# Kernel tuning notes

Measured on AMD Instinct MI355X. Metric: run time of the kernel, lower is better.

## Reference

```python
import jax, jax.numpy as jnp
import numpy as np

TEMP_LEN = 16
TARGET_LEN = 22
DIM = 768
HEADS = 12
B = 16
NT = TEMP_LEN * TEMP_LEN          # 256 template tokens
NG = TARGET_LEN * TARGET_LEN      # 484 target tokens
N = NT + NG                       # 740
POS_HID = 512


def _gaussian_heatmap(center, size, sig=1.0):
    x_axis = np.linspace(0, size[0] - 1, size[0]) - center[0]
    y_axis = np.linspace(0, size[1] - 1, size[1]) - center[1]
    xx, yy = np.meshgrid(x_axis, y_axis)
    return np.exp(-0.5 * (xx ** 2 + yy ** 2) / sig ** 2)


def _bias_index(L):
    # faithful to getBiasIndex (w_len == h_len here)
    coords = np.stack(np.meshgrid(np.arange(L), np.arange(L), indexing='ij'))  # [2,L,L]
    flat = coords.reshape(2, -1)                                               # [2,L*L]
    rel = (flat[:, :, None] - flat[:, None, :]).transpose(1, 2, 0).astype(np.int64)
    rel[:, :, 0] += L - 1
    rel[:, :, 1] += L - 1
    rel[:, :, 0] *= 2 * L - 1
    return rel.sum(-1)  # [L*L, L*L]


def setup_inputs() -> dict:
    key = jax.random.key(0)
    ks = jax.random.split(key, 12)
    f32 = jnp.float32
    x = jax.random.normal(ks[0], (B, N, DIM), dtype=f32)
    temp_q = jax.random.normal(ks[1], (B, NT, DIM), dtype=f32)
    target_q = jax.random.normal(ks[2], (B, NG, DIM), dtype=f32)
    # linear weights stored [in, out] (transposed torch layout)
    w = lambda k, i, o: jax.random.normal(k, (i, o), dtype=f32) * 0.02
    q_w = w(ks[3], DIM, DIM)
    k_w = w(ks[4], DIM, DIM)
    v_w = w(ks[5], DIM, DIM)
    proj_w = w(ks[6], DIM, DIM)
    proj_b = jnp.zeros((DIM,), dtype=f32)
    rpb_table = jax.random.normal(ks[7], ((2 * TARGET_LEN - 1) ** 2, HEADS), dtype=f32) * 0.0002
    rpb_table_temp = jax.random.normal(ks[8], ((2 * TEMP_LEN - 1) ** 2, HEADS), dtype=f32) * 0.0002
    pos_w1 = w(ks[9], 2, POS_HID)
    pos_b1 = jnp.zeros((POS_HID,), dtype=f32)
    pos_w2 = w(ks[10], POS_HID, HEADS)
    pos_b2 = jnp.zeros((HEADS,), dtype=f32)
    # deterministic cross-bias coordinate table (non-learned buffer)
    temp_tab = _gaussian_heatmap((TEMP_LEN // 2, TEMP_LEN // 2), (TEMP_LEN, TEMP_LEN)).astype(np.float32).flatten() \
        + np.linspace(-0.2, 0.2, NT, dtype=np.float32)
    targ_tab = _gaussian_heatmap((TARGET_LEN // 2, TARGET_LEN // 2), (TARGET_LEN, TARGET_LEN)).astype(np.float32).flatten() \
        + np.linspace(-0.2, 0.2, NG, dtype=np.float32)
    # torch.meshgrid default indexing='ij': [2, NT, NG] -> permute(1,2,0) -> [NT,NG,2]
    temp_target = np.stack(np.meshgrid(temp_tab, targ_tab, indexing='ij')).transpose(1, 2, 0)
    target_temp_tab = jnp.asarray(temp_target.transpose(1, 0, 2))  # [NG, NT, 2]
    temp_idx = jnp.asarray(_bias_index(TEMP_LEN))       # [NT, NT] int64
    target_idx = jnp.asarray(_bias_index(TARGET_LEN))   # [NG, NG] int64
    return {
        'x': x, 'temp_q': temp_q, 'target_q': target_q,
        'q_w': q_w, 'k_w': k_w, 'v_w': v_w, 'proj_w': proj_w, 'proj_b': proj_b,
        'rpb_table': rpb_table, 'rpb_table_temp': rpb_table_temp,
        'pos_w1': pos_w1, 'pos_b1': pos_b1, 'pos_w2': pos_w2, 'pos_b2': pos_b2,
        'target_temp_tab': target_temp_tab,
        'temp_idx': temp_idx, 'target_idx': target_idx,
    }


def reference(x, temp_q, target_q, q_w, k_w, v_w, proj_w, proj_b,
              rpb_table, rpb_table_temp, pos_w1, pos_b1, pos_w2, pos_b2,
              target_temp_tab, temp_idx, target_idx):
    Bsz, Ntok, C = x.shape
    H = HEADS
    hd = C // H
    scale = hd ** -0.5

    q_in = jnp.concatenate([temp_q, target_q], axis=1)                 # [B,N,C]
    q = (q_in @ q_w).reshape(Bsz, Ntok, H, hd).transpose(0, 2, 1, 3)   # [B,H,N,hd]
    k = (x @ k_w).reshape(Bsz, Ntok, H, hd).transpose(0, 2, 1, 3)
    v = (x @ v_w).reshape(Bsz, Ntok, H, hd).transpose(0, 2, 1, 3)

    # gathered relative position biases -> [H, Ni, Ni]
    temp_rpb = rpb_table_temp[temp_idx.reshape(-1)].reshape(NT, NT, H).transpose(2, 0, 1)
    targ_rpb = rpb_table[target_idx.reshape(-1)].reshape(NG, NG, H).transpose(2, 0, 1)
    # MLP cross bias: [NG, NT, 2] -> [NG, NT, H] -> [H, NG, NT]
    hid = jax.nn.relu(target_temp_tab @ pos_w1 + pos_b1)
    target_temp_bias = (hid @ pos_w2 + pos_b2).transpose(2, 0, 1)      # [H,NG,NT]
    temp_target_bias = target_temp_bias.transpose(0, 2, 1)             # [H,NT,NG]
    top = jnp.concatenate([temp_rpb, temp_target_bias], axis=2)        # [H,NT,N]
    bot = jnp.concatenate([target_temp_bias, targ_rpb], axis=2)        # [H,NG,N]
    bias = jnp.concatenate([top, bot], axis=1)[None]                   # [1,H,N,N]

    attn = jnp.einsum('bhnd,bhmd->bhnm', q, k) * scale + bias
    attn = jax.nn.softmax(attn, axis=-1)
    out = jnp.einsum('bhnm,bhmd->bhnd', attn, v).transpose(0, 2, 1, 3).reshape(Bsz, Ntok, C)
    return out @ proj_w + proj_b
```

## Files before the change

kernel.cpp:

```cpp
#include <hip/hip_runtime.h>


typedef unsigned short u16;
typedef short bf16x8 __attribute__((ext_vector_type(8)));
typedef float f32x4 __attribute__((ext_vector_type(4)));

#define BSZ   16
#define NTOK  740
#define NTMP  256
#define NTGT  484
#define DIMC  768
#define NHEAD 12
#define HDIM  64
#define MROWS (BSZ*NTOK)
#define LOG2E 1.44269504f
#define NEGS  (-23.0831032f)

__device__ __forceinline__ float bflo(unsigned int u) {
    return __uint_as_float(u << 16);
}
__device__ __forceinline__ float bfhi(unsigned int u) {
    return __uint_as_float(u & 0xffff0000u);
}
__device__ __forceinline__ u16 f2bf(float f) {
    unsigned int u = __float_as_uint(f);
    u += 0x7fffu + ((u >> 16) & 1u);
    return (u16)(u >> 16);
}

__device__ __forceinline__ void gl_lds16(const u16* g, u16* l) {
    __builtin_amdgcn_global_load_lds(
        (const __attribute__((address_space(1))) unsigned int*)(unsigned long long)g,
        (__attribute__((address_space(3))) unsigned int*)(unsigned int)(unsigned long long)l,
        16, 0, 0);
}

__device__ __forceinline__ size_t b2off(int h, int i, int j) {
    return ((size_t)(h * NTOK + i)) * 768 + ((j >> 6) << 6) + ((j & 15) << 2) + ((j >> 4) & 3);
}

#define PREP_MLP  484
#define PREP_TRW  (PREP_MLP + 576)
#define PREP_ALL  (PREP_TRW + 2220)

__global__ __launch_bounds__(256) void prep_kernel(
    const float* __restrict__ w0, const float* __restrict__ w1,
    const float* __restrict__ w2, const float* __restrict__ w3,
    u16* __restrict__ Wt,
    const float* __restrict__ rpb, const float* __restrict__ rpbt,
    const int* __restrict__ tidx, const int* __restrict__ gidx,
    const float* __restrict__ pw1, const float* __restrict__ pb1,
    const float* __restrict__ pw2, const float* __restrict__ pb2,
    const float* __restrict__ tab, u16* __restrict__ bias)
{
    __shared__ float T[64][65];
    const int blk = blockIdx.x;
    const int tid = threadIdx.x;

    if (blk < PREP_MLP) {
        int g = blk;
        int t = tid;
        float a  = tab[(g * NTMP + t) * 2 + 0];
        float bb = tab[(g * NTMP + t) * 2 + 1];
        float acc[NHEAD];
        #pragma unroll
        for (int h = 0; h < NHEAD; h++) acc[h] = pb2[h];
        for (int k = 0; k < 512; k++) {
            float hid = fmaxf(a * pw1[k] + bb * pw1[512 + k] + pb1[k], 0.0f);
            #pragma unroll
            for (int h = 0; h < NHEAD; h++) acc[h] += hid * pw2[k * NHEAD + h];
        }
        #pragma unroll
        for (int h = 0; h < NHEAD; h++) {
            u16 v = f2bf(acc[h] * LOG2E);
            bias[b2off(h, t, NTMP + g)] = v;
            bias[b2off(h, NTMP + g, t)] = v;
        }
    } else if (blk < PREP_TRW) {
        int t = blk - PREP_MLP;
        int z = t / 144, rem = t - z * 144;
        int bx = rem % 12, by = rem / 12;
        const float* src = (z == 0) ? w0 : (z == 1) ? w1 : (z == 2) ? w2 : w3;
        const float scale = (z == 0) ? 0.125f * LOG2E : 1.0f;
        u16* dst = Wt + (size_t)z * DIMC * DIMC;
        int out0 = bx * 64, in0 = by * 64;
        #pragma unroll
        for (int l = 0; l < 4; l++) {
            int u = tid + (l << 8);
            int r = u >> 4, c4 = (u & 15) << 2;
            float4 p = *(const float4*)(src + (size_t)(in0 + r) * DIMC + out0 + c4);
            T[r][c4] = p.x; T[r][c4 + 1] = p.y; T[r][c4 + 2] = p.z; T[r][c4 + 3] = p.w;
        }
        __syncthreads();
        #pragma unroll
        for (int l = 0; l < 2; l++) {
            int u = tid + (l << 8);
            int r = u >> 3, c8 = (u & 7) << 3;
            u16 e[8];
            #pragma unroll
            for (int i = 0; i < 8; i++) e[i] = f2bf(T[c8 + i][r] * scale);
            *(uint4*)(dst + (size_t)(out0 + r) * DIMC + in0 + c8) = *(uint4*)e;
        }
    } else {
        int t = blk - PREP_TRW;
        int jb = t % 3, i = t / 3;
        int j = jb * 256 + tid;
        u16 vals[NHEAD];
        if (j >= NTOK) {
            u16 neg = f2bf(-1e30f);
            #pragma unroll
            for (int h = 0; h < NHEAD; h++) vals[h] = neg;
        } else if (i < NTMP && j < NTMP) {
            int idx = tidx[i * NTMP + j];
            #pragma unroll
            for (int h = 0; h < NHEAD; h++) vals[h] = f2bf(rpbt[idx * NHEAD + h] * LOG2E);
        } else if (i >= NTMP && j >= NTMP) {
            int idx = gidx[(i - NTMP) * NTGT + (j - NTMP)];
            #pragma unroll
            for (int h = 0; h < NHEAD; h++) vals[h] = f2bf(rpb[idx * NHEAD + h] * LOG2E);
        } else {
            return;
        }
        #pragma unroll
        for (int h = 0; h < NHEAD; h++) bias[b2off(h, i, j)] = vals[h];
    }
}

__global__ __launch_bounds__(256) void gemm_qkv(
    const float* __restrict__ x, const float* __restrict__ tq,
    const float* __restrict__ gq, const u16* __restrict__ Wt,
    u16* __restrict__ Qo, u16* __restrict__ Ko, u16* __restrict__ Vo)
{
    __shared__ __align__(16) u16 As[4096];
    __shared__ __align__(16) u16 Bs0[8192];
    __shared__ __align__(16) u16 Bs1[8192];
    const int tid = threadIdx.x;
    const int lane = tid & 63, w = tid >> 6;
    const int quad = lane >> 4, ln = lane & 15;

    const int nwg = 12 * 185;
    const int flat = blockIdx.y * 12 + blockIdx.x;
    const int q = nwg >> 3, r = nwg & 7;
    const int xcd = flat & 7, sidx = flat >> 3;
    const int wg = (xcd < r) ? xcd * (q + 1) + sidx
                             : r * (q + 1) + (xcd - r) * q + sidx;
    const int by = wg / 12, bx = wg - by * 12;

    const int m0 = by << 6;
    const int wm = (w >> 1) << 5, wn = (w & 1) << 6;

    const int rr = tid >> 2, qq = tid & 3;
    const int arow = m0 + rr;

    if (bx < 6) {
        const int nn = bx << 7;
        const u16* Wb = Wt + (size_t)nn * DIMC;
        int b = arow / NTOK, n = arow - b * NTOK;
        const float* aptr = (n < NTMP)
                          ? tq + ((size_t)(b * NTMP + n)) * DIMC
                          : gq + ((size_t)(b * NTGT + (n - NTMP))) * DIMC;

        f32x4 acc[2][4];
        #pragma unroll
        for (int i = 0; i < 2; i++)
            #pragma unroll
            for (int j = 0; j < 4; j++) acc[i][j] = (f32x4){0.f, 0.f, 0.f, 0.f};

        #pragma unroll 1
        for (int t = 0; t < 12; t++) {
            const int k0 = t << 6;
            __syncthreads();
            const float* s = aptr + k0 + (qq << 4);
            float4 a0 = ((const float4*)s)[0], a1 = ((const float4*)s)[1];
            float4 a2 = ((const float4*)s)[2], a3 = ((const float4*)s)[3];
            #pragma unroll
            for (int l = 0; l < 4; l++) {
                int f = tid + (l << 8);
                int c8 = f >> 7, r2 = f & 127;
                gl_lds16(Wb + (size_t)r2 * DIMC + k0 + c8 * 8, &Bs0[f * 8]);
            }
            u16 e[16] = {f2bf(a0.x), f2bf(a0.y), f2bf(a0.z), f2bf(a0.w),
                         f2bf(a1.x), f2bf(a1.y), f2bf(a1.z), f2bf(a1.w),
                         f2bf(a2.x), f2bf(a2.y), f2bf(a2.z), f2bf(a2.w),
                         f2bf(a3.x), f2bf(a3.y), f2bf(a3.z), f2bf(a3.w)};
            *(uint4*)&As[(((qq << 1) + 0) * 64 + rr) * 8] = ((uint4*)e)[0];
            *(uint4*)&As[(((qq << 1) + 1) * 64 + rr) * 8] = ((uint4*)e)[1];
            __syncthreads();
            #pragma unroll
            for (int kp = 0; kp < 2; kp++) {
                bf16x8 af[2], bfr[4];
                #pragma unroll
                for (int mt = 0; mt < 2; mt++)
                    af[mt] = *(const bf16x8*)
                        &As[(((kp << 2) + quad) * 64 + wm + mt * 16 + ln) * 8];
                #pragma unroll
                for (int nt = 0; nt < 4; nt++)
                    bfr[nt] = *(const bf16x8*)
                        &Bs0[(((kp << 2) + quad) * 128 + wn + nt * 16 + ln) * 8];
                #pragma unroll
                for (int mt = 0; mt < 2; mt++)
                    #pragma unroll
                    for (int nt = 0; nt < 4; nt++)
                        acc[mt][nt] = __builtin_amdgcn_mfma_f32_16x16x32_bf16(
                            af[mt], bfr[nt], acc[mt][nt], 0, 0, 0);
            }
        }
        #pragma unroll
        for (int mt = 0; mt < 2; mt++)
            #pragma unroll
            for (int reg = 0; reg < 4; reg++) {
                int grow = m0 + wm + mt * 16 + (quad << 2) + reg;
                #pragma unroll
                for (int nt = 0; nt < 4; nt++)
                    Qo[(size_t)grow * DIMC + nn + wn + nt * 16 + ln]
                        = f2bf(acc[mt][nt][reg]);
            }
    } else {
        const int nn = (bx - 6) << 7;
        const u16* Wbk = Wt + (size_t)DIMC * DIMC + (size_t)nn * DIMC;
        const u16* Wbv = Wt + 2 * (size_t)DIMC * DIMC + (size_t)nn * DIMC;
        const float* aptr = x + (size_t)arow * DIMC;

        f32x4 ak[2][4], av[2][4];
        #pragma unroll
        for (int i = 0; i < 2; i++)
            #pragma unroll
            for (int j = 0; j < 4; j++) {
                ak[i][j] = (f32x4){0.f, 0.f, 0.f, 0.f};
                av[i][j] = (f32x4){0.f, 0.f, 0.f, 0.f};
            }

        #pragma unroll 1
        for (int t = 0; t < 12; t++) {
            const int k0 = t << 6;
            __syncthreads();
            const float* s = aptr + k0 + (qq << 4);
            float4 a0 = ((const float4*)s)[0], a1 = ((const float4*)s)[1];
            float4 a2 = ((const float4*)s)[2], a3 = ((const float4*)s)[3];
            #pragma unroll
            for (int l = 0; l < 4; l++) {
                int f = tid + (l << 8);
                int c8 = f >> 7, r2 = f & 127;
                gl_lds16(Wbk + (size_t)r2 * DIMC + k0 + c8 * 8, &Bs0[f * 8]);
                gl_lds16(Wbv + (size_t)r2 * DIMC + k0 + c8 * 8, &Bs1[f * 8]);
            }
            u16 e[16] = {f2bf(a0.x), f2bf(a0.y), f2bf(a0.z), f2bf(a0.w),
                         f2bf(a1.x), f2bf(a1.y), f2bf(a1.z), f2bf(a1.w),
                         f2bf(a2.x), f2bf(a2.y), f2bf(a2.z), f2bf(a2.w),
                         f2bf(a3.x), f2bf(a3.y), f2bf(a3.z), f2bf(a3.w)};
            *(uint4*)&As[(((qq << 1) + 0) * 64 + rr) * 8] = ((uint4*)e)[0];
            *(uint4*)&As[(((qq << 1) + 1) * 64 + rr) * 8] = ((uint4*)e)[1];
            __syncthreads();
            #pragma unroll
            for (int kp = 0; kp < 2; kp++) {
                bf16x8 af[2], bk[4], bv[4];
                #pragma unroll
                for (int mt = 0; mt < 2; mt++)
                    af[mt] = *(const bf16x8*)
                        &As[(((kp << 2) + quad) * 64 + wm + mt * 16 + ln) * 8];
                #pragma unroll
                for (int nt = 0; nt < 4; nt++) {
                    bk[nt] = *(const bf16x8*)
                        &Bs0[(((kp << 2) + quad) * 128 + wn + nt * 16 + ln) * 8];
                    bv[nt] = *(const bf16x8*)
                        &Bs1[(((kp << 2) + quad) * 128 + wn + nt * 16 + ln) * 8];
                }
                #pragma unroll
                for (int mt = 0; mt < 2; mt++)
                    #pragma unroll
                    for (int nt = 0; nt < 4; nt++) {
                        ak[mt][nt] = __builtin_amdgcn_mfma_f32_16x16x32_bf16(
                            af[mt], bk[nt], ak[mt][nt], 0, 0, 0);
                        av[mt][nt] = __builtin_amdgcn_mfma_f32_16x16x32_bf16(
                            af[mt], bv[nt], av[mt][nt], 0, 0, 0);
                    }
            }
        }
        #pragma unroll
        for (int mt = 0; mt < 2; mt++)
            #pragma unroll
            for (int reg = 0; reg < 4; reg++) {
                int grow = m0 + wm + mt * 16 + (quad << 2) + reg;
                #pragma unroll
                for (int nt = 0; nt < 4; nt++) {
                    int gcol = nn + wn + nt * 16 + ln;
                    Ko[(size_t)grow * DIMC + gcol] = f2bf(ak[mt][nt][reg]);
                    Vo[(size_t)grow * DIMC + gcol] = f2bf(av[mt][nt][reg]);
                }
            }
    }
}

__global__ __launch_bounds__(256) void gemm_proj(
    const u16* __restrict__ A, const u16* __restrict__ Wt,
    const float* __restrict__ pb, float* __restrict__ Cf)
{
    __shared__ __align__(16) u16 As[4096];
    __shared__ __align__(16) u16 Bs[8192];
    const int tid = threadIdx.x;
    const int lane = tid & 63, w = tid >> 6;
    const int quad = lane >> 4, ln = lane & 15;

    const int nwg = 6 * 185;
    const int flat = blockIdx.y * 6 + blockIdx.x;
    const int q = nwg >> 3, r = nwg & 7;
    const int xcd = flat & 7, sidx = flat >> 3;
    const int wg = (xcd < r) ? xcd * (q + 1) + sidx
                             : r * (q + 1) + (xcd - r) * q + sidx;
    const int by = wg / 6, bx = wg - by * 6;

    const int m0 = by << 6;
    const int wm = (w >> 1) << 5, wn = (w & 1) << 6;
    const int nn = bx << 7;
    const u16* Wb = Wt + (size_t)nn * DIMC;

    f32x4 acc[2][4];
    #pragma unroll
    for (int i = 0; i < 2; i++)
        #pragma unroll
        for (int j = 0; j < 4; j++) acc[i][j] = (f32x4){0.f, 0.f, 0.f, 0.f};

    #pragma unroll 1
    for (int t = 0; t < 12; t++) {
        __syncthreads();
        const int k0 = t << 6;
        #pragma unroll
        for (int l = 0; l < 2; l++) {
            int f = tid + (l << 8);
            int c8 = f >> 6, r2 = f & 63;
            gl_lds16(A + (size_t)(m0 + r2) * DIMC + k0 + c8 * 8, &As[f * 8]);
        }
        #pragma unroll
        for (int l = 0; l < 4; l++) {
            int f = tid + (l << 8);
            int c8 = f >> 7, r2 = f & 127;
            gl_lds16(Wb + (size_t)r2 * DIMC + k0 + c8 * 8, &Bs[f * 8]);
        }
        __syncthreads();
        #pragma unroll
        for (int kp = 0; kp < 2; kp++) {
            bf16x8 af[2], bfr[4];
            #pragma unroll
            for (int mt = 0; mt < 2; mt++)
                af[mt] = *(const bf16x8*)
                    &As[(((kp << 2) + quad) * 64 + wm + mt * 16 + ln) * 8];
            #pragma unroll
            for (int nt = 0; nt < 4; nt++)
                bfr[nt] = *(const bf16x8*)
                    &Bs[(((kp << 2) + quad) * 128 + wn + nt * 16 + ln) * 8];
            #pragma unroll
            for (int mt = 0; mt < 2; mt++)
                #pragma unroll
                for (int nt = 0; nt < 4; nt++)
                    acc[mt][nt] = __builtin_amdgcn_mfma_f32_16x16x32_bf16(
                        af[mt], bfr[nt], acc[mt][nt], 0, 0, 0);
        }
    }

    #pragma unroll
    for (int mt = 0; mt < 2; mt++)
        #pragma unroll
        for (int reg = 0; reg < 4; reg++) {
            int grow = m0 + wm + mt * 16 + (quad << 2) + reg;
            #pragma unroll
            for (int nt = 0; nt < 4; nt++) {
                int gcol = nn + wn + nt * 16 + ln;
                Cf[(size_t)grow * DIMC + gcol] = acc[mt][nt][reg] + pb[gcol];
            }
        }
}

__global__ __launch_bounds__(256) void attn_mfma(
    const u16* __restrict__ Qg, const u16* __restrict__ Kg,
    const u16* __restrict__ Vg, const u16* __restrict__ bias,
    u16* __restrict__ ctx)
{
    __shared__ __align__(16) u16 KsL[4096];
    __shared__ __align__(16) u16 VtL[64 * 72];
    __shared__ __align__(16) u16 Pw[4][16][72];

    const int tid = threadIdx.x;
    const int lane = tid & 63, w = tid >> 6;
    const int quad = lane >> 4, ln = lane & 15;

    const int flat = (blockIdx.z * 12 + blockIdx.y) * 12 + blockIdx.x;
    const int wg = (flat & 7) * 288 + (flat >> 3);
    const int h = wg / 192;
    const int rem = wg - h * 192;
    const int b = rem / 12;
    const int q0 = (rem - b * 12) << 6;

    const int mbase = q0 + (w << 4);
    const u16* bp = bias + ((size_t)h * NTOK) * 768;

    bf16x8 aq[2];
    {
        int qrow = mbase + ln; if (qrow >= NTOK) qrow = NTOK - 1;
        #pragma unroll
        for (int kp = 0; kp < 2; kp++)
            aq[kp] = *(const bf16x8*)(Qg + ((size_t)(b * NTOK + qrow)) * DIMC
                                      + h * HDIM + kp * 32 + (quad << 3));
    }
    int boff[4];
    #pragma unroll
    for (int reg = 0; reg < 4; reg++) {
        int rr = mbase + (quad << 2) + reg;
        if (rr >= NTOK) rr = NTOK - 1;
        boff[reg] = rr * 768 + (ln << 2);
    }

    const int pswz = ((ln >> 2) & 3) << 4;

    float rs[4] = {};
    f32x4 O[4];
    #pragma unroll
    for (int dt = 0; dt < 4; dt++) O[dt] = (f32x4){0.f, 0.f, 0.f, 0.f};

    for (int j0 = 0; j0 < NTOK; j0 += 64) {
        __syncthreads();
        #pragma unroll
        for (int l = 0; l < 2; l++) {
            int f = tid + (l << 8);
            int chunk = f >> 6, jr = f & 63;
            int krow = j0 + jr; if (krow >= NTOK) krow = NTOK - 1;
            gl_lds16(Kg + ((size_t)(b * NTOK + krow)) * DIMC + h * HDIM + chunk * 8,
                     KsL + f * 8);
        }
        uint2 bvv[4];
        #pragma unroll
        for (int reg = 0; reg < 4; reg++)
            bvv[reg] = *(const uint2*)(bp + boff[reg] + j0);
        #pragma unroll
        for (int l = 0; l < 2; l++) {
            int u = tid + (l << 8);
            int jr = u >> 3, d0 = (u & 7) << 3;
            int vrow = j0 + jr; if (vrow >= NTOK) vrow = NTOK - 1;
            uint4 p = *(const uint4*)(Vg + ((size_t)(b * NTOK + vrow)) * DIMC + h * HDIM + d0);
            const u16* pe = (const u16*)&p;
            int jswz = jr ^ d0;
            #pragma unroll
            for (int i = 0; i < 8; i++) VtL[(d0 + i) * 72 + jswz] = pe[i];
        }
        __syncthreads();

        bf16x8 bv[4][2];
        #pragma unroll
        for (int dt = 0; dt < 4; dt++) {
            int key8 = ((dt * 2 + (ln >> 3)) & 7) << 3;
            #pragma unroll
            for (int kp = 0; kp < 2; kp++) {
                int koff = (kp * 32 + (quad << 3)) ^ key8;
                bv[dt][kp] = *(const bf16x8*)&VtL[(dt * 16 + ln) * 72 + koff];
            }
        }

        f32x4 s[4];
        #pragma unroll
        for (int nt = 0; nt < 4; nt++) s[nt] = (f32x4){NEGS, NEGS, NEGS, NEGS};
        __builtin_amdgcn_s_setprio(1);
        #pragma unroll
        for (int kp = 0; kp < 2; kp++)
            #pragma unroll
            for (int nt = 0; nt < 4; nt++) {
                bf16x8 bk = *(const bf16x8*)
                    &KsL[(((kp << 2) + quad) * 64 + nt * 16 + ln) * 8];
                s[nt] = __builtin_amdgcn_mfma_f32_16x16x32_bf16(aq[kp], bk, s[nt], 0, 0, 0);
            }
        __builtin_amdgcn_s_setprio(0);

        #pragma unroll
        for (int reg = 0; reg < 4; reg++) {
            uint2 bb = bvv[reg];
            float p0 = __builtin_exp2f(s[0][reg] + bflo(bb.x));
            float p1 = __builtin_exp2f(s[1][reg] + bfhi(bb.x));
            float p2 = __builtin_exp2f(s[2][reg] + bflo(bb.y));
            float p3 = __builtin_exp2f(s[3][reg] + bfhi(bb.y));
            s[0][reg] = p0; s[1][reg] = p1;
            s[2][reg] = p2; s[3][reg] = p3;
            rs[reg] += p0 + p1 + p2 + p3;
        }
        u16* pwb = &Pw[w][0][0];
        #pragma unroll
        for (int nt = 0; nt < 4; nt++) {
            int colw = ((nt ^ quad) << 4) + ln;
            #pragma unroll
            for (int reg = 0; reg < 4; reg++)
                pwb[((quad << 2) + reg) * 72 + colw] = f2bf(s[nt][reg]);
        }
        bf16x8 ap[2];
        #pragma unroll
        for (int kp = 0; kp < 2; kp++) {
            int koff = (kp * 32 + (quad << 3)) ^ pswz;
            ap[kp] = *(const bf16x8*)&pwb[ln * 72 + koff];
        }
        __builtin_amdgcn_s_setprio(1);
        #pragma unroll
        for (int dt = 0; dt < 4; dt++)
            #pragma unroll
            for (int kp = 0; kp < 2; kp++)
                O[dt] = __builtin_amdgcn_mfma_f32_16x16x32_bf16(
                    ap[kp], bv[dt][kp], O[dt], 0, 0, 0);
        __builtin_amdgcn_s_setprio(0);
    }

    #pragma unroll
    for (int reg = 0; reg < 4; reg++) {
        float t = rs[reg];
        #pragma unroll
        for (int mk = 8; mk >= 1; mk >>= 1) t += __shfl_xor(t, mk);
        float inv = 1.0f / t;
        int row = mbase + (quad << 2) + reg;
        if (row < NTOK) {
            #pragma unroll
            for (int dt = 0; dt < 4; dt++)
                ctx[((size_t)(b * NTOK + row)) * DIMC + h * HDIM + dt * 16 + ln]
                    = f2bf(O[dt][reg] * inv);
        }
    }
}

extern "C" void kernel_launch(void* const* d_in, const int* in_sizes, int n_in,
                              void* d_out, int out_size, void* d_ws, size_t ws_size,
                              hipStream_t stream)
{
    const float* x        = (const float*)d_in[0];
    const float* temp_q   = (const float*)d_in[1];
    const float* target_q = (const float*)d_in[2];
    const float* q_w      = (const float*)d_in[3];
    const float* k_w      = (const float*)d_in[4];
    const float* v_w      = (const float*)d_in[5];
    const float* proj_w   = (const float*)d_in[6];
    const float* proj_b   = (const float*)d_in[7];
    const float* rpb      = (const float*)d_in[8];
    const float* rpbt     = (const float*)d_in[9];
    const float* pw1      = (const float*)d_in[10];
    const float* pb1      = (const float*)d_in[11];
    const float* pw2      = (const float*)d_in[12];
    const float* pb2      = (const float*)d_in[13];
    const float* tab      = (const float*)d_in[14];
    const int*   tidx     = (const int*)d_in[15];
    const int*   gidx     = (const int*)d_in[16];
    float* out = (float*)d_out;

    char* ws = (char*)d_ws;
    const size_t S = (size_t)MROWS * DIMC * sizeof(u16);
    const size_t SZB = (size_t)NHEAD * NTOK * 768 * sizeof(u16);
    u16* CTX   = (u16*)(ws);
    u16* V     = (u16*)(ws + S);
    u16* Q     = (u16*)(ws + 2 * S);
    u16* K     = (u16*)(ws + 3 * S);
    u16* BIAS2 = (u16*)(ws + 4 * S);
    u16* WT    = (u16*)(ws + 4 * S + SZB);

    prep_kernel<<<dim3(PREP_ALL), 256, 0, stream>>>(
        q_w, k_w, v_w, proj_w, WT,
        rpb, rpbt, tidx, gidx,
        pw1, pb1, pw2, pb2, tab, BIAS2);

    const u16* WTp = WT + 3 * (size_t)DIMC * DIMC;

    gemm_qkv<<<dim3(12, 185), 256, 0, stream>>>(x, temp_q, target_q, WT, Q, K, V);
    attn_mfma<<<dim3(12, 12, 16), 256, 0, stream>>>(Q, K, V, BIAS2, CTX);
    gemm_proj<<<dim3(6, 185), 256, 0, stream>>>(CTX, WTp, proj_b, out);
}
```

Measured before the change: 473.2 us.

## Split fused K/V GEMM blocks into uniform Q/K/V tiles with swizzled A LDS

The QKV projection kernel no longer has half its blocks compute both K and V. Every block now computes one 64x128 tile of Q, K or V, on an 18x185 grid. This halves the accumulators and B-tile LDS per block, adds a launch-bounds occupancy hint, and balances work across blocks. The A tile in LDS gets an XOR swizzle to cut bank conflicts. The cost is that each K/V block now reloads and reconverts the fp32 x rows that the fused version shared between K and V.

Result: no change. 470.7 us (-0.5%).

```diff
diff --git a/kernel.cpp b/kernel.cpp
--- a/kernel.cpp
+++ b/kernel.cpp
@@ -126,169 +126,104 @@
     }
 }
 
-__global__ __launch_bounds__(256) void gemm_qkv(
+__global__ __launch_bounds__(256, 6) void gemm_qkv(
     const float* __restrict__ x, const float* __restrict__ tq,
     const float* __restrict__ gq, const u16* __restrict__ Wt,
     u16* __restrict__ Qo, u16* __restrict__ Ko, u16* __restrict__ Vo)
 {
     __shared__ __align__(16) u16 As[4096];
-    __shared__ __align__(16) u16 Bs0[8192];
-    __shared__ __align__(16) u16 Bs1[8192];
+    __shared__ __align__(16) u16 Bs[8192];
     const int tid = threadIdx.x;
     const int lane = tid & 63, w = tid >> 6;
     const int quad = lane >> 4, ln = lane & 15;
 
-    const int nwg = 12 * 185;
-    const int flat = blockIdx.y * 12 + blockIdx.x;
+    const int nwg = 18 * 185;
+    const int flat = blockIdx.y * 18 + blockIdx.x;
     const int q = nwg >> 3, r = nwg & 7;
     const int xcd = flat & 7, sidx = flat >> 3;
     const int wg = (xcd < r) ? xcd * (q + 1) + sidx
                              : r * (q + 1) + (xcd - r) * q + sidx;
-    const int by = wg / 12, bx = wg - by * 12;
+    const int by = wg / 18, bx = wg - by * 18;
 
     const int m0 = by << 6;
     const int wm = (w >> 1) << 5, wn = (w & 1) << 6;
 
+    const int p = (bx < 6) ? 0 : (bx < 12) ? 1 : 2;
+    const int nn = (bx - p * 6) << 7;
+    const u16* Wb = Wt + (size_t)p * DIMC * DIMC + (size_t)nn * DIMC;
+    u16* Co = (p == 0) ? Qo : (p == 1) ? Ko : Vo;
+
     const int rr = tid >> 2, qq = tid & 3;
     const int arow = m0 + rr;
-
-    if (bx < 6) {
-        const int nn = bx << 7;
-        const u16* Wb = Wt + (size_t)nn * DIMC;
+    const float* aptr;
+    if (p == 0) {
         int b = arow / NTOK, n = arow - b * NTOK;
-        const float* aptr = (n < NTMP)
-                          ? tq + ((size_t)(b * NTMP + n)) * DIMC
-                          : gq + ((size_t)(b * NTGT + (n - NTMP))) * DIMC;
-
-        f32x4 acc[2][4];
-        #pragma unroll
-        for (int i = 0; i < 2; i++)
-            #pragma unroll
-            for (int j = 0; j < 4; j++) acc[i][j] = (f32x4){0.f, 0.f, 0.f, 0.f};
-
-        #pragma unroll 1
-        for (int t = 0; t < 12; t++) {
-            const int k0 = t << 6;
-            __syncthreads();
-            const float* s = aptr + k0 + (qq << 4);
-            float4 a0 = ((const float4*)s)[0], a1 = ((const float4*)s)[1];
-            float4 a2 = ((const float4*)s)[2], a3 = ((const float4*)s)[3];
-            #pragma unroll
-            for (int l = 0; l < 4; l++) {
-                int f = tid + (l << 8);
-                int c8 = f >> 7, r2 = f & 127;
-                gl_lds16(Wb + (size_t)r2 * DIMC + k0 + c8 * 8, &Bs0[f * 8]);
-            }
-            u16 e[16] = {f2bf(a0.x), f2bf(a0.y), f2bf(a0.z), f2bf(a0.w),
-                         f2bf(a1.x), f2bf(a1.y), f2bf(a1.z), f2bf(a1.w),
-                         f2bf(a2.x), f2bf(a2.y), f2bf(a2.z), f2bf(a2.w),
-                         f2bf(a3.x), f2bf(a3.y), f2bf(a3.z), f2bf(a3.w)};
-            *(uint4*)&As[(((qq << 1) + 0) * 64 + rr) * 8] = ((uint4*)e)[0];
-            *(uint4*)&As[(((qq << 1) + 1) * 64 + rr) * 8] = ((uint4*)e)[1];
-            __syncthreads();
-            #pragma unroll
-            for (int kp = 0; kp < 2; kp++) {
-                bf16x8 af[2], bfr[4];
-                #pragma unroll
-                for (int mt = 0; mt < 2; mt++)
-                    af[mt] = *(const bf16x8*)
-                        &As[(((kp << 2) + quad) * 64 + wm + mt * 16 + ln) * 8];
+        aptr = (n < NTMP)
+             ? tq + ((size_t)(b * NTMP + n)) * DIMC
+             : gq + ((size_t)(b * NTGT + (n - NTMP))) * DIMC;
+    } else {
+        aptr = x + (size_t)arow * DIMC;
+    }
+    const int wof0 = ((2 * qq + 0) * 64 + (rr ^ (2 * qq + 0))) * 8;
+    const int wof1 = ((2 * qq + 1) * 64 + (rr ^ (2 * qq + 1))) * 8;
+
+    f32x4 acc[2][4];
+    #pragma unroll
+    for (int i = 0; i < 2; i++)
+        #pragma unroll
+        for (int j = 0; j < 4; j++) acc[i][j] = (f32x4){0.f, 0.f, 0.f, 0.f};
+
+    #pragma unroll 1
+    for (int t = 0; t < 12; t++) {
+        const int k0 = t << 6;
+        __syncthreads();
+        const float* s = aptr + k0 + (qq << 4);
+        float4 a0 = ((const float4*)s)[0], a1 = ((const float4*)s)[1];
+        float4 a2 = ((const float4*)s)[2], a3 = ((const float4*)s)[3];
+        #pragma unroll
+        for (int l = 0; l < 4; l++) {
+            int f = tid + (l << 8);
+            int c8 = f >> 7, r2 = f & 127;
+            gl_lds16(Wb + (size_t)r2 * DIMC + k0 + c8 * 8, &Bs[f * 8]);
+        }
+        u16 e[16] = {f2bf(a0.x), f2bf(a0.y), f2bf(a0.z), f2bf(a0.w),
+                     f2bf(a1.x), f2bf(a1.y), f2bf(a1.z), f2bf(a1.w),
+                     f2bf(a2.x), f2bf(a2.y), f2bf(a2.z), f2bf(a2.w),
+                     f2bf(a3.x), f2bf(a3.y), f2bf(a3.z), f2bf(a3.w)};
+        *(uint4*)&As[wof0] = ((uint4*)e)[0];
+        *(uint4*)&As[wof1] = ((uint4*)e)[1];
+        __syncthreads();
+        #pragma unroll
+        for (int kp = 0; kp < 2; kp++) {
+            const int kc0 = (kp << 2) + quad;
+            bf16x8 af[2], bfr[4];
+            #pragma unroll
+            for (int mt = 0; mt < 2; mt++)
+                af[mt] = *(const bf16x8*)
+                    &As[(kc0 * 64 + wm + mt * 16 + (ln ^ kc0)) * 8];
+            #pragma unroll
+            for (int nt = 0; nt < 4; nt++)
+                bfr[nt] = *(const bf16x8*)
+                    &Bs[(kc0 * 128 + wn + nt * 16 + ln) * 8];
+            #pragma unroll
+            for (int mt = 0; mt < 2; mt++)
                 #pragma unroll
                 for (int nt = 0; nt < 4; nt++)
-                    bfr[nt] = *(const bf16x8*)
-                        &Bs0[(((kp << 2) + quad) * 128 + wn + nt * 16 + ln) * 8];
-                #pragma unroll
-                for (int mt = 0; mt < 2; mt++)
-                    #pragma unroll
-                    for (int nt = 0; nt < 4; nt++)
-                        acc[mt][nt] = __builtin_amdgcn_mfma_f32_16x16x32_bf16(
-                            af[mt], bfr[nt], acc[mt][nt], 0, 0, 0);
-            }
-        }
-        #pragma unroll
-        for (int mt = 0; mt < 2; mt++)
-            #pragma unroll
-            for (int reg = 0; reg < 4; reg++) {
-                int grow = m0 + wm + mt * 16 + (quad << 2) + reg;
-                #pragma unroll
-                for (int nt = 0; nt < 4; nt++)
-                    Qo[(size_t)grow * DIMC + nn + wn + nt * 16 + ln]
-                        = f2bf(acc[mt][nt][reg]);
-            }
-    } else {
-        const int nn = (bx - 6) << 7;
-        const u16* Wbk = Wt + (size_t)DIMC * DIMC + (size_t)nn * DIMC;
-        const u16* Wbv = Wt + 2 * (size_t)DIMC * DIMC + (size_t)nn * DIMC;
-        const float* aptr = x + (size_t)arow * DIMC;
-
-        f32x4 ak[2][4], av[2][4];
-        #pragma unroll
-        for (int i = 0; i < 2; i++)
-            #pragma unroll
-            for (int j = 0; j < 4; j++) {
-                ak[i][j] = (f32x4){0.f, 0.f, 0.f, 0.f};
-                av[i][j] = (f32x4){0.f, 0.f, 0.f, 0.f};
-            }
-
-        #pragma unroll 1
-        for (int t = 0; t < 12; t++) {
-            const int k0 = t << 6;
-            __syncthreads();
-            const float* s = aptr + k0 + (qq << 4);
-            float4 a0 = ((const float4*)s)[0], a1 = ((const float4*)s)[1];
-            float4 a2 = ((const float4*)s)[2], a3 = ((const float4*)s)[3];
-            #pragma unroll
-            for (int l = 0; l < 4; l++) {
-                int f = tid + (l << 8);
-                int c8 = f >> 7, r2 = f & 127;
-                gl_lds16(Wbk + (size_t)r2 * DIMC + k0 + c8 * 8, &Bs0[f * 8]);
-                gl_lds16(Wbv + (size_t)r2 * DIMC + k0 + c8 * 8, &Bs1[f * 8]);
-            }
-            u16 e[16] = {f2bf(a0.x), f2bf(a0.y), f2bf(a0.z), f2bf(a0.w),
-                         f2bf(a1.x), f2bf(a1.y), f2bf(a1.z), f2bf(a1.w),
-                         f2bf(a2.x), f2bf(a2.y), f2bf(a2.z), f2bf(a2.w),
-                         f2bf(a3.x), f2bf(a3.y), f2bf(a3.z), f2bf(a3.w)};
-            *(uint4*)&As[(((qq << 1) + 0) * 64 + rr) * 8] = ((uint4*)e)[0];
-            *(uint4*)&As[(((qq << 1) + 1) * 64 + rr) * 8] = ((uint4*)e)[1];
-            __syncthreads();
-            #pragma unroll
-            for (int kp = 0; kp < 2; kp++) {
-                bf16x8 af[2], bk[4], bv[4];
-                #pragma unroll
-                for (int mt = 0; mt < 2; mt++)
-                    af[mt] = *(const bf16x8*)
-                        &As[(((kp << 2) + quad) * 64 + wm + mt * 16 + ln) * 8];
-                #pragma unroll
-                for (int nt = 0; nt < 4; nt++) {
-                    bk[nt] = *(const bf16x8*)
-                        &Bs0[(((kp << 2) + quad) * 128 + wn + nt * 16 + ln) * 8];
-                    bv[nt] = *(const bf16x8*)
-                        &Bs1[(((kp << 2) + quad) * 128 + wn + nt * 16 + ln) * 8];
-                }
-                #pragma unroll
-                for (int mt = 0; mt < 2; mt++)
-                    #pragma unroll
-                    for (int nt = 0; nt < 4; nt++) {
-                        ak[mt][nt] = __builtin_amdgcn_mfma_f32_16x16x32_bf16(
-                            af[mt], bk[nt], ak[mt][nt], 0, 0, 0);
-                        av[mt][nt] = __builtin_amdgcn_mfma_f32_16x16x32_bf16(
-                            af[mt], bv[nt], av[mt][nt], 0, 0, 0);
-                    }
-            }
-        }
-        #pragma unroll
-        for (int mt = 0; mt < 2; mt++)
-            #pragma unroll
-            for (int reg = 0; reg < 4; reg++) {
-                int grow = m0 + wm + mt * 16 + (quad << 2) + reg;
-                #pragma unroll
-                for (int nt = 0; nt < 4; nt++) {
-                    int gcol = nn + wn + nt * 16 + ln;
-                    Ko[(size_t)grow * DIMC + gcol] = f2bf(ak[mt][nt][reg]);
-                    Vo[(size_t)grow * DIMC + gcol] = f2bf(av[mt][nt][reg]);
-                }
-            }
-    }
+                    acc[mt][nt] = __builtin_amdgcn_mfma_f32_16x16x32_bf16(
+                        af[mt], bfr[nt], acc[mt][nt], 0, 0, 0);
+        }
+    }
+
+    #pragma unroll
+    for (int mt = 0; mt < 2; mt++)
+        #pragma unroll
+        for (int reg = 0; reg < 4; reg++) {
+            int grow = m0 + wm + mt * 16 + (quad << 2) + reg;
+            #pragma unroll
+            for (int nt = 0; nt < 4; nt++)
+                Co[(size_t)grow * DIMC + nn + wn + nt * 16 + ln]
+                    = f2bf(acc[mt][nt][reg]);
+        }
 }
 
 __global__ __launch_bounds__(256) void gemm_proj(
@@ -559,7 +494,7 @@
 
     const u16* WTp = WT + 3 * (size_t)DIMC * DIMC;
 
-    gemm_qkv<<<dim3(12, 185), 256, 0, stream>>>(x, temp_q, target_q, WT, Q, K, V);
+    gemm_qkv<<<dim3(18, 185), 256, 0, stream>>>(x, temp_q, target_q, WT, Q, K, V);
     attn_mfma<<<dim3(12, 12, 16), 256, 0, stream>>>(Q, K, V, BIAS2, CTX);
     gemm_proj<<<dim3(6, 185), 256, 0, stream>>>(CTX, WTp, proj_b, out);
 }
```
